# Kernel optimization log

Hardware: AMD Instinct MI355X
Metric: run time of the kernel (lower is better)

The kernel has to match this reference:

```python
import jax, jax.numpy as jnp
import numpy as np

NUM_BINS = 10
HIST_RANGE = 10.0
LN_EPS = 1e-5
NUM_SERVERS = 64
START_IDX = 2 + 2 + NUM_SERVERS  # = 68


def layer_norm(x, g, b):
    mu = jnp.mean(x, axis=-1, keepdims=True)
    var = jnp.mean(jnp.square(x - mu), axis=-1, keepdims=True)
    return (x - mu) * jax.lax.rsqrt(var + LN_EPS) * g + b


def batched_histogram(w):
    # w: [B, S]; replicates np.histogram(w_i, bins=10, range=(0,10)) per row,
    # then normalizes by (sum + 1e-8). Values outside [0,10] are excluded;
    # value == 10 falls in the last bin.
    idx = jnp.clip(jnp.floor(w * (NUM_BINS / HIST_RANGE)).astype(jnp.int32), 0, NUM_BINS - 1)
    mask = ((w >= 0.0) & (w <= HIST_RANGE)).astype(w.dtype)
    oh = jax.nn.one_hot(idx, NUM_BINS, dtype=w.dtype) * mask[..., None]  # [B,S,NB]
    hist = jnp.sum(oh, axis=1)  # [B,NB]
    return hist / (jnp.sum(hist, axis=-1, keepdims=True) + 1e-8)


def setup_inputs() -> dict:
    key = jax.random.key(0)
    ks = jax.random.split(key, 16)
    B, OBS, ACT, H, NB = 65536, 512, 64, 128, NUM_BINS
    COMB = (OBS - NUM_SERVERS) + 128 + 64  # 640

    def lin(k, fin, fout):
        bound = 1.0 / np.sqrt(fin)
        kw, kb = jax.random.split(k)
        return (jax.random.uniform(kw, (fin, fout), jnp.float32, -bound, bound),
                jax.random.uniform(kb, (fout,), jnp.float32, -bound, bound))

    obs = jax.random.uniform(ks[0], (B, OBS), jnp.float32, 0.0, 10.0)
    preference = jax.random.uniform(ks[1], (B, 2), jnp.float32)
    h_w1, h_b1 = lin(ks[2], NB, H)
    h_w2, h_b2 = lin(ks[3], H, H)
    p_w, p_b = lin(ks[4], 2, 64)
    s_w1, s_b1 = lin(ks[5], COMB, 256)
    s_w2, s_b2 = lin(ks[6], 256, 256)
    qd_w, qd_b = lin(ks[7], 256, ACT)
    qe_w, qe_b = lin(ks[8], 256, ACT)
    return {
        'obs': obs, 'preference': preference,
        'h_w1': h_w1, 'h_b1': h_b1,
        'h_ln1_g': jnp.ones((H,)), 'h_ln1_b': jnp.zeros((H,)),
        'h_w2': h_w2, 'h_b2': h_b2,
        'h_ln2_g': jnp.ones((H,)), 'h_ln2_b': jnp.zeros((H,)),
        'p_w': p_w, 'p_b': p_b,
        'p_ln_g': jnp.ones((64,)), 'p_ln_b': jnp.zeros((64,)),
        's_w1': s_w1, 's_b1': s_b1,
        's_ln1_g': jnp.ones((256,)), 's_ln1_b': jnp.zeros((256,)),
        's_w2': s_w2, 's_b2': s_b2,
        's_ln2_g': jnp.ones((256,)), 's_ln2_b': jnp.zeros((256,)),
        'qd_w': qd_w, 'qd_b': qd_b, 'qe_w': qe_w, 'qe_b': qe_b,
    }


def reference(obs, preference,
              h_w1, h_b1, h_ln1_g, h_ln1_b, h_w2, h_b2, h_ln2_g, h_ln2_b,
              p_w, p_b, p_ln_g, p_ln_b,
              s_w1, s_b1, s_ln1_g, s_ln1_b, s_w2, s_b2, s_ln2_g, s_ln2_b,
              qd_w, qd_b, qe_w, qe_b):
    server_workloads = obs[:, START_IDX:START_IDX + NUM_SERVERS]
    obs_wo = jnp.concatenate([obs[:, :START_IDX], obs[:, START_IDX + NUM_SERVERS:]], axis=-1)

    hist = batched_histogram(server_workloads)  # [B, 10]
    h = layer_norm(jax.nn.relu(hist @ h_w1 + h_b1), h_ln1_g, h_ln1_b)
    h = layer_norm(jax.nn.relu(h @ h_w2 + h_b2), h_ln2_g, h_ln2_b)  # [B,128]

    p = layer_norm(jax.nn.relu(preference @ p_w + p_b), p_ln_g, p_ln_b)  # [B,64]

    combined = jnp.concatenate([obs_wo, h, p], axis=-1)  # [B,640]
    s = layer_norm(jax.nn.relu(combined @ s_w1 + s_b1), s_ln1_g, s_ln1_b)
    s = layer_norm(jax.nn.relu(s @ s_w2 + s_b2), s_ln2_g, s_ln2_b)  # [B,256]

    q_delay = s @ qd_w + qd_b   # [B,A]
    q_energy = s @ qe_w + qe_b  # [B,A]
    return jnp.stack([q_delay, q_energy], axis=-1)  # [B,A,2]
```

## Files before the change

kernel.cpp:

```cpp
#include <hip/hip_runtime.h>

typedef __bf16 bf16x8 __attribute__((ext_vector_type(8)));
typedef __bf16 bf16x4 __attribute__((ext_vector_type(4)));
typedef float  f32x4  __attribute__((ext_vector_type(4)));

#define OFF_W1  0
#define OFF_W2  163840
#define OFF_WQ  229376
#define OFF_WH1 262144
#define OFF_WH2 266240
#define WS_ELEMS 282624

__global__ __launch_bounds__(256) void prep_kernel(
    const float* __restrict__ s_w1, const float* __restrict__ s_w2,
    const float* __restrict__ qd_w, const float* __restrict__ qe_w,
    const float* __restrict__ h_w1, const float* __restrict__ h_w2,
    __bf16* __restrict__ wsb)
{
  int idx = blockIdx.x * 256 + threadIdx.x;
  if (idx >= WS_ELEMS) return;
  float val = 0.f;
  if (idx < OFF_W2) {
    int t = idx;
    int j = t & 7, l = (t >> 3) & 63, rest = t >> 9;
    int nt = rest & 15, ks = rest >> 4;
    int k = ks * 32 + (l >> 4) * 8 + j, n = nt * 16 + (l & 15);
    val = s_w1[k * 256 + n];
  } else if (idx < OFF_WQ) {
    int t = idx - OFF_W2;
    int j = t & 7, l = (t >> 3) & 63, rest = t >> 9;
    int nt = rest & 15, ks = rest >> 4;
    int k = ks * 32 + (l >> 4) * 8 + j, n = nt * 16 + (l & 15);
    val = s_w2[k * 256 + n];
  } else if (idx < OFF_WH1) {
    int t = idx - OFF_WQ;
    int j = t & 7, l = (t >> 3) & 63, rest = t >> 9;
    int nt = rest & 7, ks = rest >> 3;
    int k = ks * 32 + (l >> 4) * 8 + j, n = nt * 16 + (l & 15);
    int a = n >> 1;
    val = (n & 1) ? qe_w[k * 64 + a] : qd_w[k * 64 + a];
  } else if (idx < OFF_WH2) {
    int t = idx - OFF_WH1;
    int j = t & 7, l = (t >> 3) & 63, rest = t >> 9;
    int nt = rest & 7;
    int k = (l >> 4) * 8 + j, n = nt * 16 + (l & 15);
    val = (k < 10) ? h_w1[k * 128 + n] : 0.f;
  } else {
    int t = idx - OFF_WH2;
    int j = t & 7, l = (t >> 3) & 63, rest = t >> 9;
    int nt = rest & 7, ks = rest >> 3;
    int k = ks * 32 + (l >> 4) * 8 + j, n = nt * 16 + (l & 15);
    val = h_w2[k * 128 + n];
  }
  wsb[idx] = (__bf16)val;
}

template<int CTRL>
__device__ __forceinline__ float dppadd(float x) {
  int p = __builtin_amdgcn_mov_dpp(__float_as_int(x), CTRL, 0xF, 0xF, true);
  return x + __int_as_float(p);
}
__device__ __forceinline__ float row16_reduce(float x) {
  x = dppadd<0x121>(x);
  x = dppadd<0x122>(x);
  x = dppadd<0x124>(x);
  x = dppadd<0x128>(x);
  return x;
}

template<int KSTEPS, int NT_TOT, int NTW>
__device__ __forceinline__ void run_gemm(const __bf16* A, int astride,
    const bf16x8* __restrict__ Bsw, int wave, int lane, f32x4 acc[NTW])
{
  const int quad = lane >> 4, ln = lane & 15;
  const int ntb = wave * NTW;
  bf16x8 bcur[NTW];
#pragma unroll
  for (int i = 0; i < NTW; ++i) bcur[i] = Bsw[(ntb + i) * 64 + lane];
#pragma unroll
  for (int ks = 0; ks < KSTEPS; ++ks) {
    bf16x8 bnxt[NTW];
    if (ks + 1 < KSTEPS) {
#pragma unroll
      for (int i = 0; i < NTW; ++i)
        bnxt[i] = Bsw[((ks + 1) * NT_TOT + ntb + i) * 64 + lane];
    }
    bf16x8 a = *(const bf16x8*)(A + ln * astride + ks * 32 + quad * 8);
#pragma unroll
    for (int i = 0; i < NTW; ++i)
      acc[i] = __builtin_amdgcn_mfma_f32_16x16x32_bf16(a, bcur[i], acc[i], 0, 0, 0);
    if (ks + 1 < KSTEPS) {
#pragma unroll
      for (int i = 0; i < NTW; ++i) bcur[i] = bnxt[i];
    }
  }
}

template<int W, int NTW>
__device__ __forceinline__ void epilogue_ln(f32x4 acc[NTW],
    const float* __restrict__ bias, const float* __restrict__ g, const float* __restrict__ bb,
    __bf16* Adst, int dstride, int dstcol0,
    float2* red, int wave, int lane)
{
  const int quad = lane >> 4, ln = lane & 15;
  float x[NTW][4];
#pragma unroll
  for (int i = 0; i < NTW; ++i) {
    int n = (wave * NTW + i) * 16 + ln;
    float b = bias[n];
#pragma unroll
    for (int r = 0; r < 4; ++r)
      x[i][r] = fmaxf(acc[i][r] + b, 0.f);
  }
  float s[4] = {0, 0, 0, 0}, q[4] = {0, 0, 0, 0};
#pragma unroll
  for (int i = 0; i < NTW; ++i)
#pragma unroll
    for (int r = 0; r < 4; ++r) { s[r] += x[i][r]; q[r] += x[i][r] * x[i][r]; }
#pragma unroll
  for (int r = 0; r < 4; ++r) {
    s[r] = row16_reduce(s[r]);
    q[r] = row16_reduce(q[r]);
  }
  if (ln == 0) {
#pragma unroll
    for (int r = 0; r < 4; ++r)
      red[wave * 16 + quad * 4 + r] = make_float2(s[r], q[r]);
  }
  __syncthreads();
#pragma unroll
  for (int r = 0; r < 4; ++r) {
    int m = quad * 4 + r;
    float tot = 0.f, totq = 0.f;
#pragma unroll
    for (int w2 = 0; w2 < 8; ++w2) {
      float2 t = red[w2 * 16 + m];
      tot += t.x; totq += t.y;
    }
    float mu = tot / (float)W;
    float var = totq / (float)W - mu * mu;
    float rs = rsqrtf(var + 1e-5f);
#pragma unroll
    for (int i = 0; i < NTW; ++i) {
      int n = (wave * NTW + i) * 16 + ln;
      float o = (x[i][r] - mu) * rs * g[n] + bb[n];
      Adst[m * dstride + dstcol0 + n] = (__bf16)o;
    }
  }
  __syncthreads();
}

__global__ __launch_bounds__(512, 8) void critic_kernel(
    const float* __restrict__ obs, const float* __restrict__ pref,
    const float* __restrict__ h_b1, const float* __restrict__ h_g1, const float* __restrict__ h_bb1,
    const float* __restrict__ h_b2, const float* __restrict__ h_g2, const float* __restrict__ h_bb2,
    const float* __restrict__ p_w, const float* __restrict__ p_b,
    const float* __restrict__ p_g, const float* __restrict__ p_bb,
    const float* __restrict__ s_b1, const float* __restrict__ s_g1, const float* __restrict__ s_bb1,
    const float* __restrict__ s_b2, const float* __restrict__ s_g2, const float* __restrict__ s_bb2,
    const float* __restrict__ qd_b, const float* __restrict__ qe_b,
    const __bf16* __restrict__ wsb, float* __restrict__ out)
{
  __shared__ __align__(16) __bf16 A_comb[16 * 648];
  __shared__ __align__(16) __bf16 A_s[16 * 264];
  __shared__ __align__(16) __bf16 A_h[16 * 40];
  __shared__ float2 red[128];

  const int tid = threadIdx.x;
  const int wave = tid >> 6, lane = tid & 63;
  const int rowbase = blockIdx.x * 16;

  float pw0 = p_w[lane], pw1 = p_w[64 + lane], pb = p_b[lane];
  float pg = p_g[lane], pbb = p_bb[lane];
#pragma unroll
  for (int r = 0; r < 2; ++r) {
    int row = wave * 2 + r;
    int grow = rowbase + row;
    const float* orow = obs + (size_t)grow * 512;
#pragma unroll
    for (int j = 0; j < 2; ++j) {
      int l = lane + 64 * j;
      if (l < 112) {
        int src4 = (l < 17) ? l : l + 16;
        float4 v = *(const float4*)(orow + 4 * src4);
        bf16x4 o;
        o[0] = (__bf16)v.x; o[1] = (__bf16)v.y; o[2] = (__bf16)v.z; o[3] = (__bf16)v.w;
        *(bf16x4*)(&A_comb[row * 648 + 4 * l]) = o;
      }
    }
    float w = orow[68 + lane];
    int bi = (int)floorf(w);
    bi = bi < 0 ? 0 : (bi > 9 ? 9 : bi);
    bool valid = (w >= 0.f) && (w <= 10.f);
    float tot = 0.f, mine = 0.f;
#pragma unroll
    for (int b = 0; b < 10; ++b) {
      unsigned long long mk = __ballot(valid && (bi == b));
      float c = (float)__popcll(mk);
      tot += c;
      if (lane == b) mine = c;
    }
    float inv = 1.f / (tot + 1e-8f);
    if (lane < 32) A_h[row * 40 + lane] = (__bf16)((lane < 10) ? mine * inv : 0.f);
    float a0 = pref[grow * 2], a1 = pref[grow * 2 + 1];
    float v = fmaxf(fmaf(a0, pw0, fmaf(a1, pw1, pb)), 0.f);
    float s1 = v, s2 = v * v;
    s1 = row16_reduce(s1); s2 = row16_reduce(s2);
    s1 += __shfl_xor(s1, 16, 64); s2 += __shfl_xor(s2, 16, 64);
    s1 += __shfl_xor(s1, 32, 64); s2 += __shfl_xor(s2, 32, 64);
    float mu = s1 * (1.f / 64.f);
    float var = s2 * (1.f / 64.f) - mu * mu;
    float o = (v - mu) * rsqrtf(var + 1e-5f) * pg + pbb;
    A_comb[row * 648 + 576 + lane] = (__bf16)o;
  }
  __syncthreads();

  {
    f32x4 acc[1] = {};
    run_gemm<1, 8, 1>(A_h, 40, (const bf16x8*)(wsb + OFF_WH1), wave, lane, acc);
    epilogue_ln<128, 1>(acc, h_b1, h_g1, h_bb1, A_s, 264, 0, red, wave, lane);
  }
  {
    f32x4 acc[1] = {};
    run_gemm<4, 8, 1>(A_s, 264, (const bf16x8*)(wsb + OFF_WH2), wave, lane, acc);
    epilogue_ln<128, 1>(acc, h_b2, h_g2, h_bb2, A_comb, 648, 448, red, wave, lane);
  }
  {
    f32x4 acc[2] = {};
    run_gemm<20, 16, 2>(A_comb, 648, (const bf16x8*)(wsb + OFF_W1), wave, lane, acc);
    epilogue_ln<256, 2>(acc, s_b1, s_g1, s_bb1, A_s, 264, 0, red, wave, lane);
  }
  {
    f32x4 acc[2] = {};
    run_gemm<8, 16, 2>(A_s, 264, (const bf16x8*)(wsb + OFF_W2), wave, lane, acc);
    epilogue_ln<256, 2>(acc, s_b2, s_g2, s_bb2, A_s, 264, 0, red, wave, lane);
  }
  {
    f32x4 acc[1] = {};
    run_gemm<8, 8, 1>(A_s, 264, (const bf16x8*)(wsb + OFF_WQ), wave, lane, acc);
    const int quad = lane >> 4, ln = lane & 15;
    int n = wave * 16 + ln;
    float qb = (n & 1) ? qe_b[n >> 1] : qd_b[n >> 1];
#pragma unroll
    for (int r = 0; r < 4; ++r) {
      int m = quad * 4 + r;
      out[(size_t)(rowbase + m) * 128 + n] = acc[0][r] + qb;
    }
  }
}

extern "C" void kernel_launch(void* const* d_in, const int* in_sizes, int n_in,
                              void* d_out, int out_size, void* d_ws, size_t ws_size,
                              hipStream_t stream) {
  const float* obs    = (const float*)d_in[0];
  const float* pref   = (const float*)d_in[1];
  const float* h_w1   = (const float*)d_in[2];
  const float* h_b1   = (const float*)d_in[3];
  const float* h_g1   = (const float*)d_in[4];
  const float* h_bb1  = (const float*)d_in[5];
  const float* h_w2   = (const float*)d_in[6];
  const float* h_b2   = (const float*)d_in[7];
  const float* h_g2   = (const float*)d_in[8];
  const float* h_bb2  = (const float*)d_in[9];
  const float* p_w    = (const float*)d_in[10];
  const float* p_b    = (const float*)d_in[11];
  const float* p_g    = (const float*)d_in[12];
  const float* p_bb   = (const float*)d_in[13];
  const float* s_w1   = (const float*)d_in[14];
  const float* s_b1   = (const float*)d_in[15];
  const float* s_g1   = (const float*)d_in[16];
  const float* s_bb1  = (const float*)d_in[17];
  const float* s_w2   = (const float*)d_in[18];
  const float* s_b2   = (const float*)d_in[19];
  const float* s_g2   = (const float*)d_in[20];
  const float* s_bb2  = (const float*)d_in[21];
  const float* qd_w   = (const float*)d_in[22];
  const float* qd_b   = (const float*)d_in[23];
  const float* qe_w   = (const float*)d_in[24];
  const float* qe_b   = (const float*)d_in[25];

  __bf16* wsb = (__bf16*)d_ws;
  int B = in_sizes[0] / 512;
  int nblocks = B / 16;

  prep_kernel<<<(WS_ELEMS + 255) / 256, 256, 0, stream>>>(s_w1, s_w2, qd_w, qe_w, h_w1, h_w2, wsb);
  critic_kernel<<<nblocks, 512, 0, stream>>>(
      obs, pref, h_b1, h_g1, h_bb1, h_b2, h_g2, h_bb2,
      p_w, p_b, p_g, p_bb, s_b1, s_g1, s_bb1, s_b2, s_g2, s_bb2,
      qd_b, qe_b, (const __bf16*)wsb, (float*)d_out);
}
```

Before: 350.5 us.

## Fold LayerNorm affine and normalization into following GEMM weights and epilogues

Folds the LayerNorm gamma into the next layer's weights and precomputes the correction vectors c = g·W and e = bb·W + b in a small prep kernel. The raw ReLU activations now go to shared memory right away, and each LN is applied after the next GEMM as rs*(acc - mu*c) + e. Row statistics are accumulated with LDS atomics into per-layer slots, which removes one barrier and the second LDS pass per epilogue. This reorders the numerics: raw activations are quantized to bf16 before normalization, and variance uses E[x^2]-mu^2, so accuracy may drift. It also adds an extra prep launch.

```diff
diff --git a/kernel.cpp b/kernel.cpp
--- a/kernel.cpp
+++ b/kernel.cpp
@@ -10,11 +10,19 @@
 #define OFF_WH1 262144
 #define OFF_WH2 266240
 #define WS_ELEMS 282624
+#define CE_CH2 0
+#define CE_EH2 128
+#define CE_C2  256
+#define CE_E2  512
+#define CE_CQ  768
+#define CE_EQ  896
 
 __global__ __launch_bounds__(256) void prep_kernel(
     const float* __restrict__ s_w1, const float* __restrict__ s_w2,
     const float* __restrict__ qd_w, const float* __restrict__ qe_w,
     const float* __restrict__ h_w1, const float* __restrict__ h_w2,
+    const float* __restrict__ h_g1, const float* __restrict__ s_g1,
+    const float* __restrict__ s_g2,
     __bf16* __restrict__ wsb)
 {
   int idx = blockIdx.x * 256 + threadIdx.x;
@@ -31,14 +39,14 @@
     int j = t & 7, l = (t >> 3) & 63, rest = t >> 9;
     int nt = rest & 15, ks = rest >> 4;
     int k = ks * 32 + (l >> 4) * 8 + j, n = nt * 16 + (l & 15);
-    val = s_w2[k * 256 + n];
+    val = s_w2[k * 256 + n] * s_g1[k];
   } else if (idx < OFF_WH1) {
     int t = idx - OFF_WQ;
     int j = t & 7, l = (t >> 3) & 63, rest = t >> 9;
     int nt = rest & 7, ks = rest >> 3;
     int k = ks * 32 + (l >> 4) * 8 + j, n = nt * 16 + (l & 15);
     int a = n >> 1;
-    val = (n & 1) ? qe_w[k * 64 + a] : qd_w[k * 64 + a];
+    val = ((n & 1) ? qe_w[k * 64 + a] : qd_w[k * 64 + a]) * s_g2[k];
   } else if (idx < OFF_WH2) {
     int t = idx - OFF_WH1;
     int j = t & 7, l = (t >> 3) & 63, rest = t >> 9;
@@ -50,9 +58,54 @@
     int j = t & 7, l = (t >> 3) & 63, rest = t >> 9;
     int nt = rest & 7, ks = rest >> 3;
     int k = ks * 32 + (l >> 4) * 8 + j, n = nt * 16 + (l & 15);
-    val = h_w2[k * 128 + n];
+    val = h_w2[k * 128 + n] * h_g1[k];
   }
   wsb[idx] = (__bf16)val;
+}
+
+__global__ __launch_bounds__(256) void prep_ce(
+    const float* __restrict__ h_w2, const float* __restrict__ h_g1,
+    const float* __restrict__ h_bb1, const float* __restrict__ h_b2,
+    const float* __restrict__ s_w2, const float* __restrict__ s_g1,
+    const float* __restrict__ s_bb1, const float* __restrict__ s_b2,
+    const float* __restrict__ qd_w, const float* __restrict__ qe_w,
+    const float* __restrict__ s_g2, const float* __restrict__ s_bb2,
+    const float* __restrict__ qd_b, const float* __restrict__ qe_b,
+    float* __restrict__ ce)
+{
+  int t = blockIdx.x * 256 + threadIdx.x;
+  if (t < 128) {
+    float s = 0.f;
+    for (int k = 0; k < 128; ++k) s += h_g1[k] * h_w2[k * 128 + t];
+    ce[CE_CH2 + t] = s;
+  } else if (t < 256) {
+    int n = t - 128;
+    float s = h_b2[n];
+    for (int k = 0; k < 128; ++k) s += h_bb1[k] * h_w2[k * 128 + n];
+    ce[t] = s;
+  } else if (t < 512) {
+    int n = t - 256;
+    float s = 0.f;
+    for (int k = 0; k < 256; ++k) s += s_g1[k] * s_w2[k * 256 + n];
+    ce[t] = s;
+  } else if (t < 768) {
+    int n = t - 512;
+    float s = s_b2[n];
+    for (int k = 0; k < 256; ++k) s += s_bb1[k] * s_w2[k * 256 + n];
+    ce[t] = s;
+  } else if (t < 896) {
+    int n = t - 768, a = n >> 1;
+    const float* W = (n & 1) ? qe_w : qd_w;
+    float s = 0.f;
+    for (int k = 0; k < 256; ++k) s += s_g2[k] * W[k * 64 + a];
+    ce[t] = s;
+  } else if (t < 1024) {
+    int n = t - 896, a = n >> 1;
+    const float* W = (n & 1) ? qe_w : qd_w;
+    float s = (n & 1) ? qe_b[a] : qd_b[a];
+    for (int k = 0; k < 256; ++k) s += s_bb2[k] * W[k * 64 + a];
+    ce[t] = s;
+  }
 }
 
 template<int CTRL>
@@ -68,6 +121,41 @@
   return x;
 }
 
+__device__ __forceinline__ void slot_stats(const float* slot, float invW, int quad,
+                                           float mu[4], float rs[4]) {
+  f32x4 v0 = *(const f32x4*)(slot + quad * 8);
+  f32x4 v1 = *(const f32x4*)(slot + quad * 8 + 4);
+  float ts[4] = {v0[0], v0[2], v1[0], v1[2]};
+  float tq[4] = {v0[1], v0[3], v1[1], v1[3]};
+#pragma unroll
+  for (int r = 0; r < 4; ++r) {
+    mu[r] = ts[r] * invW;
+    float var = tq[r] * invW - mu[r] * mu[r];
+    rs[r] = rsqrtf(var + 1e-5f);
+  }
+}
+
+template<int NTW>
+__device__ __forceinline__ void reduce_slot(float x[NTW][4], float* slot, int lane) {
+  const int quad = lane >> 4, ln = lane & 15;
+  float s[4] = {0, 0, 0, 0}, q[4] = {0, 0, 0, 0};
+#pragma unroll
+  for (int i = 0; i < NTW; ++i)
+#pragma unroll
+    for (int r = 0; r < 4; ++r) { s[r] += x[i][r]; q[r] += x[i][r] * x[i][r]; }
+#pragma unroll
+  for (int r = 0; r < 4; ++r) { s[r] = row16_reduce(s[r]); q[r] = row16_reduce(q[r]); }
+  if (ln == 0) {
+#pragma unroll
+    for (int r = 0; r < 4; ++r) {
+      int m = quad * 4 + r;
+      atomicAdd(&slot[2 * m], s[r]);
+      atomicAdd(&slot[2 * m + 1], q[r]);
+    }
+  }
+  __syncthreads();
+}
+
 template<int KSTEPS, int NT_TOT, int NTW>
 __device__ __forceinline__ void run_gemm(const __bf16* A, int astride,
     const bf16x8* __restrict__ Bsw, int wave, int lane, f32x4 acc[NTW])
@@ -96,11 +184,11 @@
   }
 }
 
-template<int W, int NTW>
-__device__ __forceinline__ void epilogue_ln(f32x4 acc[NTW],
-    const float* __restrict__ bias, const float* __restrict__ g, const float* __restrict__ bb,
+template<int NTW>
+__device__ __forceinline__ void epilogue_raw(f32x4 acc[NTW],
+    const float* __restrict__ bias,
     __bf16* Adst, int dstride, int dstcol0,
-    float2* red, int wave, int lane)
+    float* slot, int wave, int lane)
 {
   const int quad = lane >> 4, ln = lane & 15;
   float x[NTW][4];
@@ -109,66 +197,60 @@
     int n = (wave * NTW + i) * 16 + ln;
     float b = bias[n];
 #pragma unroll
-    for (int r = 0; r < 4; ++r)
+    for (int r = 0; r < 4; ++r) {
       x[i][r] = fmaxf(acc[i][r] + b, 0.f);
-  }
-  float s[4] = {0, 0, 0, 0}, q[4] = {0, 0, 0, 0};
-#pragma unroll
-  for (int i = 0; i < NTW; ++i)
-#pragma unroll
-    for (int r = 0; r < 4; ++r) { s[r] += x[i][r]; q[r] += x[i][r] * x[i][r]; }
-#pragma unroll
-  for (int r = 0; r < 4; ++r) {
-    s[r] = row16_reduce(s[r]);
-    q[r] = row16_reduce(q[r]);
-  }
-  if (ln == 0) {
-#pragma unroll
-    for (int r = 0; r < 4; ++r)
-      red[wave * 16 + quad * 4 + r] = make_float2(s[r], q[r]);
-  }
-  __syncthreads();
-#pragma unroll
-  for (int r = 0; r < 4; ++r) {
-    int m = quad * 4 + r;
-    float tot = 0.f, totq = 0.f;
-#pragma unroll
-    for (int w2 = 0; w2 < 8; ++w2) {
-      float2 t = red[w2 * 16 + m];
-      tot += t.x; totq += t.y;
-    }
-    float mu = tot / (float)W;
-    float var = totq / (float)W - mu * mu;
-    float rs = rsqrtf(var + 1e-5f);
-#pragma unroll
-    for (int i = 0; i < NTW; ++i) {
-      int n = (wave * NTW + i) * 16 + ln;
-      float o = (x[i][r] - mu) * rs * g[n] + bb[n];
-      Adst[m * dstride + dstcol0 + n] = (__bf16)o;
-    }
-  }
-  __syncthreads();
+      Adst[(quad * 4 + r) * dstride + dstcol0 + n] = (__bf16)x[i][r];
+    }
+  }
+  reduce_slot<NTW>(x, slot, lane);
+}
+
+template<int NTW>
+__device__ __forceinline__ void epilogue_fold_raw(f32x4 acc[NTW],
+    const float* __restrict__ cvec, const float* __restrict__ evec,
+    const float* __restrict__ slot_prev, float invWprev,
+    __bf16* Adst, int dstride, int dstcol0,
+    float* slot, int wave, int lane)
+{
+  const int quad = lane >> 4, ln = lane & 15;
+  float mu[4], rs[4];
+  slot_stats(slot_prev, invWprev, quad, mu, rs);
+  float x[NTW][4];
+#pragma unroll
+  for (int i = 0; i < NTW; ++i) {
+    int n = (wave * NTW + i) * 16 + ln;
+    float c = cvec[n], e = evec[n];
+#pragma unroll
+    for (int r = 0; r < 4; ++r) {
+      float z = fmaf(rs[r], fmaf(-mu[r], c, acc[i][r]), e);
+      x[i][r] = fmaxf(z, 0.f);
+      Adst[(quad * 4 + r) * dstride + dstcol0 + n] = (__bf16)x[i][r];
+    }
+  }
+  reduce_slot<NTW>(x, slot, lane);
 }
 
 __global__ __launch_bounds__(512, 8) void critic_kernel(
     const float* __restrict__ obs, const float* __restrict__ pref,
-    const float* __restrict__ h_b1, const float* __restrict__ h_g1, const float* __restrict__ h_bb1,
-    const float* __restrict__ h_b2, const float* __restrict__ h_g2, const float* __restrict__ h_bb2,
+    const float* __restrict__ h_b1,
+    const float* __restrict__ h_g2, const float* __restrict__ h_bb2,
     const float* __restrict__ p_w, const float* __restrict__ p_b,
     const float* __restrict__ p_g, const float* __restrict__ p_bb,
-    const float* __restrict__ s_b1, const float* __restrict__ s_g1, const float* __restrict__ s_bb1,
-    const float* __restrict__ s_b2, const float* __restrict__ s_g2, const float* __restrict__ s_bb2,
-    const float* __restrict__ qd_b, const float* __restrict__ qe_b,
-    const __bf16* __restrict__ wsb, float* __restrict__ out)
+    const float* __restrict__ s_b1,
+    const __bf16* __restrict__ wsb, const float* __restrict__ ce,
+    float* __restrict__ out)
 {
   __shared__ __align__(16) __bf16 A_comb[16 * 648];
   __shared__ __align__(16) __bf16 A_s[16 * 264];
   __shared__ __align__(16) __bf16 A_h[16 * 40];
-  __shared__ float2 red[128];
+  __shared__ __align__(16) float red4[4][32];
 
   const int tid = threadIdx.x;
   const int wave = tid >> 6, lane = tid & 63;
   const int rowbase = blockIdx.x * 16;
+  __bf16* X2 = A_comb;
+
+  if (tid < 128) ((float*)red4)[tid] = 0.f;
 
   float pw0 = p_w[lane], pw1 = p_w[64 + lane], pb = p_b[lane];
   float pg = p_g[lane], pbb = p_bb[lane];
@@ -218,33 +300,56 @@
   {
     f32x4 acc[1] = {};
     run_gemm<1, 8, 1>(A_h, 40, (const bf16x8*)(wsb + OFF_WH1), wave, lane, acc);
-    epilogue_ln<128, 1>(acc, h_b1, h_g1, h_bb1, A_s, 264, 0, red, wave, lane);
+    epilogue_raw<1>(acc, h_b1, A_s, 264, 0, red4[0], wave, lane);
   }
   {
     f32x4 acc[1] = {};
     run_gemm<4, 8, 1>(A_s, 264, (const bf16x8*)(wsb + OFF_WH2), wave, lane, acc);
-    epilogue_ln<128, 1>(acc, h_b2, h_g2, h_bb2, A_comb, 648, 448, red, wave, lane);
+    const int quad = lane >> 4, ln = lane & 15;
+    float mu0[4], rs0[4];
+    slot_stats(red4[0], 1.f / 128.f, quad, mu0, rs0);
+    int n = wave * 16 + ln;
+    float c = ce[CE_CH2 + n], e = ce[CE_EH2 + n];
+    float x[1][4];
+#pragma unroll
+    for (int r = 0; r < 4; ++r) {
+      float z = fmaf(rs0[r], fmaf(-mu0[r], c, acc[0][r]), e);
+      x[0][r] = fmaxf(z, 0.f);
+    }
+    reduce_slot<1>(x, red4[1], lane);
+    float mu[4], rs[4];
+    slot_stats(red4[1], 1.f / 128.f, quad, mu, rs);
+    float gg = h_g2[n], bv = h_bb2[n];
+#pragma unroll
+    for (int r = 0; r < 4; ++r) {
+      float o = (x[0][r] - mu[r]) * rs[r] * gg + bv;
+      A_comb[(quad * 4 + r) * 648 + 448 + n] = (__bf16)o;
+    }
+    __syncthreads();
   }
   {
     f32x4 acc[2] = {};
     run_gemm<20, 16, 2>(A_comb, 648, (const bf16x8*)(wsb + OFF_W1), wave, lane, acc);
-    epilogue_ln<256, 2>(acc, s_b1, s_g1, s_bb1, A_s, 264, 0, red, wave, lane);
+    epilogue_raw<2>(acc, s_b1, A_s, 264, 0, red4[2], wave, lane);
   }
   {
     f32x4 acc[2] = {};
     run_gemm<8, 16, 2>(A_s, 264, (const bf16x8*)(wsb + OFF_W2), wave, lane, acc);
-    epilogue_ln<256, 2>(acc, s_b2, s_g2, s_bb2, A_s, 264, 0, red, wave, lane);
+    epilogue_fold_raw<2>(acc, ce + CE_C2, ce + CE_E2, red4[2], 1.f / 256.f,
+                         X2, 264, 0, red4[3], wave, lane);
   }
   {
     f32x4 acc[1] = {};
-    run_gemm<8, 8, 1>(A_s, 264, (const bf16x8*)(wsb + OFF_WQ), wave, lane, acc);
+    run_gemm<8, 8, 1>(X2, 264, (const bf16x8*)(wsb + OFF_WQ), wave, lane, acc);
     const int quad = lane >> 4, ln = lane & 15;
+    float mu[4], rs[4];
+    slot_stats(red4[3], 1.f / 256.f, quad, mu, rs);
     int n = wave * 16 + ln;
-    float qb = (n & 1) ? qe_b[n >> 1] : qd_b[n >> 1];
+    float c = ce[CE_CQ + n], e = ce[CE_EQ + n];
 #pragma unroll
     for (int r = 0; r < 4; ++r) {
       int m = quad * 4 + r;
-      out[(size_t)(rowbase + m) * 128 + n] = acc[0][r] + qb;
+      out[(size_t)(rowbase + m) * 128 + n] = fmaf(rs[r], fmaf(-mu[r], c, acc[0][r]), e);
     }
   }
 }
@@ -280,12 +385,16 @@
   const float* qe_b   = (const float*)d_in[25];
 
   __bf16* wsb = (__bf16*)d_ws;
+  float* ce = (float*)(wsb + WS_ELEMS);
   int B = in_sizes[0] / 512;
   int nblocks = B / 16;
 
-  prep_kernel<<<(WS_ELEMS + 255) / 256, 256, 0, stream>>>(s_w1, s_w2, qd_w, qe_w, h_w1, h_w2, wsb);
+  prep_kernel<<<(WS_ELEMS + 255) / 256, 256, 0, stream>>>(
+      s_w1, s_w2, qd_w, qe_w, h_w1, h_w2, h_g1, s_g1, s_g2, wsb);
+  prep_ce<<<4, 256, 0, stream>>>(
+      h_w2, h_g1, h_bb1, h_b2, s_w2, s_g1, s_bb1, s_b2,
+      qd_w, qe_w, s_g2, s_bb2, qd_b, qe_b, ce);
   critic_kernel<<<nblocks, 512, 0, stream>>>(
-      obs, pref, h_b1, h_g1, h_bb1, h_b2, h_g2, h_bb2,
-      p_w, p_b, p_g, p_bb, s_b1, s_g1, s_bb1, s_b2, s_g2, s_bb2,
-      qd_b, qe_b, (const __bf16*)wsb, (float*)d_out);
-}
+      obs, pref, h_b1, h_g2, h_bb2, p_w, p_b, p_g, p_bb, s_b1,
+      (const __bf16*)wsb, (const float*)ce, (float*)d_out);
+}
```

New measurement: 346.5 us. Within noise of the previous version (-1.1%).
